# Optimization experiments

Hardware: AMD Instinct MI355X
Metric: run time of the kernel (lower is better)

The kernel has to match this reference:

```python
import jax, jax.numpy as jnp
import numpy as np

N_NODES = 20000
N_EDGES = 640000
NODE_NF = 64
HIDDEN = 256
N_LAYERS = 4


def _linear_init(key, fan_in, fan_out, layers=None):
    shape = (fan_in, fan_out) if layers is None else (layers, fan_in, fan_out)
    scale = 1.0 / np.sqrt(fan_in)
    return jax.random.normal(key, shape, dtype=jnp.float32) * scale


def setup_inputs() -> dict:
    key = jax.random.key(0)
    ks = jax.random.split(key, 16)
    L, H = N_LAYERS, HIDDEN
    return {
        "h": jax.random.normal(ks[0], (N_NODES, NODE_NF), dtype=jnp.float32),
        "edge_index": jax.random.randint(ks[1], (2, N_EDGES), 0, N_NODES, dtype=jnp.int64),
        "coord_diff": jax.random.normal(ks[2], (N_EDGES, 3), dtype=jnp.float32),
        # embedding in / out
        "w_in": _linear_init(ks[3], NODE_NF, H),
        "b_in": jnp.zeros((H,), jnp.float32),
        "w_out": _linear_init(ks[4], H, NODE_NF),
        "b_out": jnp.zeros((NODE_NF,), jnp.float32),
        # per-layer edge MLP: Linear(2H+1 -> H), silu, Linear(H -> H), silu
        "edge_w1": _linear_init(ks[5], 2 * H + 1, H, L),
        "edge_b1": jnp.zeros((L, H), jnp.float32),
        "edge_w2": _linear_init(ks[6], H, H, L),
        "edge_b2": jnp.zeros((L, H), jnp.float32),
        # per-layer node MLP: Linear(2H -> H), silu, Linear(H -> H)
        "node_w1": _linear_init(ks[7], 2 * H, H, L),
        "node_b1": jnp.zeros((L, H), jnp.float32),
        "node_w2": _linear_init(ks[8], H, H, L),
        "node_b2": jnp.zeros((L, H), jnp.float32),
    }


def reference(h, edge_index, coord_diff, w_in, b_in, w_out, b_out,
              edge_w1, edge_b1, edge_w2, edge_b2,
              node_w1, node_b1, node_w2, node_b2):
    row, col = edge_index[0], edge_index[1]
    # radial is layer-independent: [E, 1]
    radial = jnp.sum(coord_diff ** 2, axis=1, keepdims=True)

    h = h @ w_in + b_in  # [N, H]
    n_nodes = h.shape[0]

    for l in range(N_LAYERS):
        # edge model: gather endpoints, concat with radial, 2-layer MLP
        m = jnp.concatenate([h[row], h[col], radial], axis=1)  # [E, 2H+1]
        m = jax.nn.silu(m @ edge_w1[l] + edge_b1[l])
        m = jax.nn.silu(m @ edge_w2[l] + edge_b2[l])  # [E, H]
        # node model: segment-sum aggregate over row, concat, 2-layer MLP
        agg = jax.ops.segment_sum(m, row, num_segments=n_nodes)  # [N, H]
        x = jnp.concatenate([h, agg], axis=1)  # [N, 2H]
        x = jax.nn.silu(x @ node_w1[l] + node_b1[l])
        h = x @ node_w2[l] + node_b2[l]  # recurrent=False: no residual

    return h @ w_out + b_out  # [N, node_nf]
```

## Files before the change

### kernel.cpp

```cpp
#include <hip/hip_runtime.h>
#include <hip/hip_bf16.h>
#include <cstdint>
#include <cstddef>

#define NN 20000
#define NE 640000
#define NF 64
#define HD 256
#define NL 4
#define HTS 640

typedef __attribute__((ext_vector_type(8))) short short8;
typedef __attribute__((ext_vector_type(4))) float f32x4;
typedef __attribute__((ext_vector_type(2))) float f32x2;

__device__ __forceinline__ float bf2f(unsigned short u){
  union { unsigned int i; float f; } x; x.i = ((unsigned int)u) << 16; return x.f;
}
__device__ __forceinline__ unsigned short f2bf(float f){
  union { float f; unsigned int i; } x; x.f = f;
  unsigned int r = x.i + 0x7FFFu + ((x.i >> 16) & 1u);
  return (unsigned short)(r >> 16);
}
__device__ __forceinline__ unsigned int pk2bf(float a, float b){
  union { __hip_bfloat162 h; unsigned int u; } cv;
  cv.h = __float22bfloat162_rn(float2{a, b});
  return cv.u;
}
__device__ __forceinline__ float silu_f(float v){
  float e = __builtin_amdgcn_exp2f(v * -1.442695041f);
  return v * __builtin_amdgcn_rcpf(1.0f + e);
}
__device__ __forceinline__ f32x2 silu2(f32x2 v){
  f32x2 t = v * (f32x2){-1.442695041f, -1.442695041f};
  f32x2 e = (f32x2){__builtin_amdgcn_exp2f(t.x), __builtin_amdgcn_exp2f(t.y)};
  f32x2 d = e + (f32x2){1.0f, 1.0f};
  f32x2 r = (f32x2){__builtin_amdgcn_rcpf(d.x), __builtin_amdgcn_rcpf(d.y)};
  return v * r;
}
__device__ __forceinline__ void async16(const void* g, void* l){
  __builtin_amdgcn_global_load_lds(
      (const __attribute__((address_space(1))) unsigned int*)g,
      (__attribute__((address_space(3))) unsigned int*)l, 16, 0, 0);
}

__global__ __launch_bounds__(256) void prep_small(
    const float* __restrict__ w_in, const float* __restrict__ w_out,
    const float* __restrict__ ew1, const float* __restrict__ ew2,
    const float* __restrict__ nw1, const float* __restrict__ nw2,
    const float* __restrict__ eb1,
    unsigned short* __restrict__ w_in_t, unsigned short* __restrict__ w_out_t,
    unsigned short* __restrict__ ew1cat, float* __restrict__ w1r,
    float* __restrict__ b1e,
    unsigned short* __restrict__ ew2t, unsigned short* __restrict__ nw1t,
    unsigned short* __restrict__ nw2t)
{
  const int s = blockIdx.y;
  const int tid = blockIdx.x * 256 + threadIdx.x;
  if (s == 18) {
    if (tid < NL * 512) {
      int l = tid >> 9, c = tid & 511;
      b1e[tid] = (c < 256) ? eb1[l * HD + c] : 0.0f;
    }
    return;
  }
  if (s >= 2 && s < 6) {
    int l = s - 2;
    if (tid >= 513 * HD) return;
    int k = tid / HD, n = tid - k * HD;
    float v = ew1[(size_t)l * 513 * HD + tid];
    if (k == 512) { w1r[l * HD + n] = v; return; }
    unsigned short* dst = ew1cat + (size_t)l * 512 * 256;
    if (k < 256) dst[(size_t)n * 256 + k] = f2bf(v);
    else         dst[(size_t)(256 + n) * 256 + (k - 256)] = f2bf(v);
    return;
  }
  const float* src; unsigned short* dst; int K, N;
  if (s == 0)      { src = w_in;  dst = w_in_t;  K = NF;   N = HD; }
  else if (s == 1) { src = w_out; dst = w_out_t; K = HD;   N = NF; }
  else if (s < 10) { int l = s-6;  src = ew2 + (size_t)l*HD*HD;   dst = ew2t + (size_t)l*HD*HD;  K = HD;   N = HD; }
  else if (s < 14) { int l = s-10; src = nw1 + (size_t)l*2*HD*HD; dst = nw1t + (size_t)l*HD*512; K = 2*HD; N = HD; }
  else             { int l = s-14; src = nw2 + (size_t)l*HD*HD;   dst = nw2t + (size_t)l*HD*HD;  K = HD;   N = HD; }
  if (tid >= K * N) return;
  int k = tid / N, n = tid - k * N;
  dst[(size_t)n * K + k] = f2bf(src[tid]);
}

__global__ __launch_bounds__(256) void prep_big(
    const float* __restrict__ h_in, const float* __restrict__ cd,
    unsigned short* __restrict__ hb_in, float* __restrict__ radial)
{
  const int s = blockIdx.y;
  const int tid = blockIdx.x * 256 + threadIdx.x;
  if (s == 0) {
    if (tid < NN * NF) hb_in[tid] = f2bf(h_in[tid]);
  } else {
    if (tid < NE) {
      float x = cd[tid*3+0], y = cd[tid*3+1], z = cd[tid*3+2];
      radial[tid] = x*x + y*y + z*z;
    }
  }
}

__global__ __launch_bounds__(256) void hist_k(const int* __restrict__ erow, int* __restrict__ hist){
  int e = blockIdx.x * 256 + threadIdx.x;
  if (e < NE){
    unsigned r = (unsigned)erow[e]; if (r >= NN) r = 0;
    atomicAdd(&hist[r], 1);
  }
}

__global__ __launch_bounds__(256) void scan_k(const int* __restrict__ hist,
                                              int* __restrict__ starts, int* __restrict__ cursor){
  __shared__ int part[256];
  const int t = threadIdx.x;
  const int CH = 79;
  int lo = t * CH, hi = lo + CH; if (hi > NN) hi = NN; if (lo > NN) lo = NN;
  int s = 0;
  for (int i = lo; i < hi; ++i) s += hist[i];
  part[t] = s; __syncthreads();
  for (int off = 1; off < 256; off <<= 1){
    int v = (t >= off) ? part[t - off] : 0;
    __syncthreads();
    part[t] += v;
    __syncthreads();
  }
  int base = (t == 0) ? 0 : part[t - 1];
  for (int i = lo; i < hi; ++i){ starts[i] = base; cursor[i] = base; base += hist[i]; }
  if (t == 255) starts[NN] = part[255];
}

__global__ __launch_bounds__(256) void scatter_k(const int* __restrict__ erow,
                                                 const int* __restrict__ ecol,
                                                 const float* __restrict__ radial,
                                                 int* __restrict__ cursor,
                                                 int* __restrict__ rowcol,
                                                 float* __restrict__ radial_s){
  int e = blockIdx.x * 256 + threadIdx.x;
  if (e < NE){
    unsigned r = (unsigned)erow[e]; if (r >= NN) r = 0;
    unsigned c = (unsigned)ecol[e]; if (c >= NN) c = 0;
    int pos = atomicAdd(&cursor[r], 1);
    rowcol[2*pos]   = (int)r;
    rowcol[2*pos+1] = (int)c;
    radial_s[pos] = radial[e];
  }
}

__global__ __launch_bounds__(256) void gemm_k(
    const unsigned short* __restrict__ Am, const unsigned short* __restrict__ Wt,
    const float* __restrict__ bias,
    unsigned short* __restrict__ outB, float* __restrict__ outF,
    unsigned short* __restrict__ outB2,
    int M, int N, int K, int lda, int ldc, int fuseSilu)
{
  __shared__ __align__(16) unsigned short As[128*32];
  __shared__ __align__(16) unsigned short Bs[128*32];
  const int t = threadIdx.x;
  const int lane = t & 63, wave = t >> 6;
  const int ln15 = lane & 15, q = lane >> 4;
  const int bm = blockIdx.x, bn = blockIdx.y;
  const int wm = wave >> 1, wn = wave & 1;

  f32x4 acc[4][4];
  #pragma unroll
  for (int i = 0; i < 4; ++i)
    #pragma unroll
    for (int j = 0; j < 4; ++j) acc[i][j] = (f32x4){0.f,0.f,0.f,0.f};

  const int sr = t >> 2;
  const int sc = (t & 3) * 8;
  int am0 = bm*128 + sr;      if (am0 > M-1) am0 = M-1;
  int am1 = bm*128 + 64 + sr; if (am1 > M-1) am1 = M-1;
  int an0 = bn*128 + sr;      if (an0 > N-1) an0 = N-1;
  int an1 = bn*128 + 64 + sr; if (an1 > N-1) an1 = N-1;
  const unsigned short* a0 = Am + (size_t)am0 * lda + sc;
  const unsigned short* a1 = Am + (size_t)am1 * lda + sc;
  const unsigned short* b0 = Wt + (size_t)an0 * K + sc;
  const unsigned short* b1 = Wt + (size_t)an1 * K + sc;

  const int nkt = K >> 5;
  for (int kt = 0; kt < nkt; ++kt) {
    const int k0 = kt * 32;
    async16(a0 + k0, &As[t*8]);
    async16(a1 + k0, &As[2048 + t*8]);
    async16(b0 + k0, &Bs[t*8]);
    async16(b1 + k0, &Bs[2048 + t*8]);
    __syncthreads();
    short8 fa[4], fb[4];
    #pragma unroll
    for (int i = 0; i < 4; ++i)
      fa[i] = *(const short8*)&As[(wm*64 + i*16 + ln15)*32 + q*8];
    #pragma unroll
    for (int j = 0; j < 4; ++j)
      fb[j] = *(const short8*)&Bs[(wn*64 + j*16 + ln15)*32 + q*8];
    #pragma unroll
    for (int i = 0; i < 4; ++i)
      #pragma unroll
      for (int j = 0; j < 4; ++j)
        acc[i][j] = __builtin_amdgcn_mfma_f32_16x16x32_bf16(fa[i], fb[j], acc[i][j], 0, 0, 0);
    __syncthreads();
  }

  #pragma unroll
  for (int i = 0; i < 4; ++i) {
    #pragma unroll
    for (int j = 0; j < 4; ++j) {
      const int n = bn*128 + wn*64 + j*16 + ln15;
      if (n >= N) continue;
      const float bv = bias ? bias[n] : 0.0f;
      #pragma unroll
      for (int r = 0; r < 4; ++r) {
        const int m = bm*128 + wm*64 + i*16 + q*4 + r;
        if (m >= M) continue;
        float v = acc[i][j][r] + bv;
        if (fuseSilu) v = silu_f(v);
        if (outB) {
          unsigned short b = f2bf(v);
          outB[(size_t)m * ldc + n] = b;
          if (outB2 && n < 256) outB2[(size_t)m * 512 + n] = b;
        }
        else outF[(size_t)m * ldc + n] = v;
      }
    }
  }
}

__global__ __launch_bounds__(256, 4) void edge_k(
    const unsigned short* __restrict__ hT,
    const int* __restrict__ rowcol,
    const float* __restrict__ radial_s,
    const float* __restrict__ w1r,
    const unsigned short* __restrict__ w2t,
    const float* __restrict__ b2,
    float* __restrict__ agg)
{
  __shared__ __align__(16) unsigned short MBUF[16896];
  __shared__ int   rowS[64];
  __shared__ float w1rS[256];
  unsigned short* M1  = MBUF;
  unsigned short* m2T = MBUF;

  const int t = threadIdx.x;
  const int lane = t & 63, wave = t >> 6;
  const int ln15 = lane & 15, q = lane >> 4;
  int blk = blockIdx.x;
  blk = (blk & 7) * ((int)gridDim.x >> 3) + (blk >> 3);
  const int e0 = blk * 64;
  const int sr = t >> 2;
  const int sc_swz = (((t & 3) ^ ((sr >> 1) & 3))) * 8;
  const int xq = ((q ^ ((ln15 >> 1) & 3))) * 8;

  const int2 rc = *(const int2*)(rowcol + 2*(e0 + sr));
  int rowv = 0;
  if (t < 64) rowv = rowcol[2*(e0 + t)];
  const float w1v = w1r[t];
  const float rad = radial_s[e0 + sr];

  float bv2[4];
  #pragma unroll
  for (int j = 0; j < 4; ++j) bv2[j] = b2[wave*64 + j*16 + ln15];

  const unsigned short* hr = hT + (size_t)rc.x * HTS + sc_swz;
  const unsigned short* hc = hT + (size_t)rc.y * HTS + 256 + sc_swz;

  short8 va[8], vb[8];
  #pragma unroll
  for (int ch = 0; ch < 8; ++ch) {
    va[ch] = *(const short8*)(hr + ch*32);
    vb[ch] = *(const short8*)(hc + ch*32);
  }

  if (t < 64) rowS[t] = rowv;
  w1rS[t] = w1v;

  const unsigned short* w2row[4];
  #pragma unroll
  for (int j = 0; j < 4; ++j)
    w2row[j] = w2t + (size_t)(wave*64 + j*16 + ln15) * HD + q*8;

  __syncthreads();

  const f32x2 rad2 = (f32x2){rad, rad};
  #pragma unroll
  for (int ch = 0; ch < 8; ++ch) {
    const int c0 = ch*32 + sc_swz;
    const unsigned int* ua = (const unsigned int*)&va[ch];
    const unsigned int* ub = (const unsigned int*)&vb[ch];
    union { unsigned int u[4]; short8 s; } res;
    #pragma unroll
    for (int i = 0; i < 4; ++i) {
      union { unsigned int i; float f; } alo, ahi, blo, bhi;
      alo.i = ua[i] << 16; ahi.i = ua[i] & 0xFFFF0000u;
      blo.i = ub[i] << 16; bhi.i = ub[i] & 0xFFFF0000u;
      f32x2 av = (f32x2){alo.f, ahi.f};
      f32x2 bv = (f32x2){blo.f, bhi.f};
      f32x2 wv = *(const f32x2*)&w1rS[c0 + 2*i];
      f32x2 o = av + bv;
      o = o + rad2 * wv;
      f32x2 sv = silu2(o);
      res.u[i] = pk2bf(sv.x, sv.y);
    }
    *(short8*)&M1[ch*2048 + sr*32 + (t & 3)*8] = res.s;
  }
  __syncthreads();

  f32x4 acc2[4][4];
  #pragma unroll
  for (int i = 0; i < 4; ++i)
    #pragma unroll
    for (int j = 0; j < 4; ++j) acc2[i][j] = (f32x4){0.f,0.f,0.f,0.f};

  __builtin_amdgcn_s_setprio(1);
  #pragma unroll
  for (int kt = 0; kt < 8; ++kt) {
    short8 fa[4], fb[4];
    #pragma unroll
    for (int j = 0; j < 4; ++j) fb[j] = *(const short8*)(w2row[j] + kt*32);
    #pragma unroll
    for (int i = 0; i < 4; ++i) fa[i] = *(const short8*)&M1[kt*2048 + (i*16 + ln15)*32 + xq];
    #pragma unroll
    for (int i = 0; i < 4; ++i)
      #pragma unroll
      for (int j = 0; j < 4; ++j)
        acc2[i][j] = __builtin_amdgcn_mfma_f32_16x16x32_bf16(fa[i], fb[j], acc2[i][j], 0, 0, 0);
  }
  __builtin_amdgcn_s_setprio(0);
  __syncthreads();

  #pragma unroll
  for (int i = 0; i < 4; ++i) {
    #pragma unroll
    for (int j = 0; j < 4; ++j) {
      const int n = wave*64 + j*16 + ln15;
      const f32x2 b2v = (f32x2){bv2[j], bv2[j]};
      f32x2 s01 = (f32x2){acc2[i][j][0], acc2[i][j][1]} + b2v;
      f32x2 s23 = (f32x2){acc2[i][j][2], acc2[i][j][3]} + b2v;
      f32x2 r01 = silu2(s01);
      f32x2 r23 = silu2(s23);
      const int m = i*16 + q*4;
      *(unsigned int*)&m2T[n*66 + m]     = pk2bf(r01.x, r01.y);
      *(unsigned int*)&m2T[n*66 + m + 2] = pk2bf(r23.x, r23.y);
    }
  }
  __syncthreads();

  {
    const int c = t;
    int cur = __builtin_amdgcn_readfirstlane(rowS[0]);
    float s = 0.f;
    #pragma unroll
    for (int m = 0; m < 64; m += 4) {
      unsigned int u0 = *(const unsigned int*)&m2T[c*66 + m];
      unsigned int u1 = *(const unsigned int*)&m2T[c*66 + m + 2];
      int n0 = __builtin_amdgcn_readfirstlane(rowS[m]);
      int n1 = __builtin_amdgcn_readfirstlane(rowS[m+1]);
      int n2 = __builtin_amdgcn_readfirstlane(rowS[m+2]);
      int n3 = __builtin_amdgcn_readfirstlane(rowS[m+3]);
      float f0 = bf2f((unsigned short)u0), f1 = bf2f((unsigned short)(u0 >> 16));
      float f2v = bf2f((unsigned short)u1), f3 = bf2f((unsigned short)(u1 >> 16));
      if (n0 != cur) { atomicAdd(&agg[(size_t)cur * HD + c], s); s = 0.f; cur = n0; }
      s += f0;
      if (n1 != cur) { atomicAdd(&agg[(size_t)cur * HD + c], s); s = 0.f; cur = n1; }
      s += f1;
      if (n2 != cur) { atomicAdd(&agg[(size_t)cur * HD + c], s); s = 0.f; cur = n2; }
      s += f2v;
      if (n3 != cur) { atomicAdd(&agg[(size_t)cur * HD + c], s); s = 0.f; cur = n3; }
      s += f3;
    }
    atomicAdd(&agg[(size_t)cur * HD + c], s);
  }
}

__global__ __launch_bounds__(256) void aggcvt_k(
    float* __restrict__ agg, unsigned short* __restrict__ xcat)
{
  const int g = blockIdx.x * 256 + threadIdx.x;
  const int node = g >> 6;
  const int c = (g & 63) * 4;
  if (node >= NN) return;
  float4 a = *(const float4*)(agg + (size_t)node * HD + c);
  uint2 pk; pk.x = pk2bf(a.x, a.y); pk.y = pk2bf(a.z, a.w);
  *(uint2*)(xcat + (size_t)node * 2 * HD + HD + c) = pk;
  *(float4*)(agg + (size_t)node * HD + c) = float4{0.f, 0.f, 0.f, 0.f};
}

extern "C" void kernel_launch(void* const* d_in, const int* in_sizes, int n_in,
                              void* d_out, int out_size, void* d_ws, size_t ws_size,
                              hipStream_t stream)
{
  (void)in_sizes; (void)n_in; (void)out_size; (void)ws_size;
  const float* h_in  = (const float*)d_in[0];
  const int*   ei    = (const int*)d_in[1];
  const float* cd    = (const float*)d_in[2];
  const float* w_in  = (const float*)d_in[3];
  const float* b_in  = (const float*)d_in[4];
  const float* w_out = (const float*)d_in[5];
  const float* b_out = (const float*)d_in[6];
  const float* ew1   = (const float*)d_in[7];
  const float* eb1   = (const float*)d_in[8];
  const float* ew2   = (const float*)d_in[9];
  const float* eb2   = (const float*)d_in[10];
  const float* nw1   = (const float*)d_in[11];
  const float* nb1   = (const float*)d_in[12];
  const float* nw2   = (const float*)d_in[13];
  const float* nb2   = (const float*)d_in[14];
  float* out = (float*)d_out;

  char* base = (char*)d_ws;
  size_t off = 0;
  auto WS = [&](size_t bytes) -> char* {
    char* p = base + off;
    off = (off + bytes + 255) & ~(size_t)255;
    return p;
  };
  float*          radial  = (float*)WS((size_t)NE * 4);
  unsigned short* hb_in   = (unsigned short*)WS((size_t)NN * NF * 2);
  unsigned short* hcur    = (unsigned short*)WS((size_t)NN * HD * 2);
  unsigned short* xcat    = (unsigned short*)WS((size_t)NN * 2 * HD * 2);
  float*          aggF    = (float*)WS((size_t)NN * HD * 4);
  unsigned short* hT      = (unsigned short*)WS((size_t)NN * HTS * 2);
  unsigned short* x1      = hT;
  unsigned short* w_in_t  = (unsigned short*)WS((size_t)NF * HD * 2);
  unsigned short* w_out_t = (unsigned short*)WS((size_t)NF * HD * 2);
  unsigned short* ew1cat  = (unsigned short*)WS((size_t)NL * 512 * 256 * 2);
  float*          w1r     = (float*)WS((size_t)NL * HD * 4);
  float*          b1e     = (float*)WS((size_t)NL * 512 * 4);
  unsigned short* ew2t    = (unsigned short*)WS((size_t)NL * HD * HD * 2);
  unsigned short* nw1t    = (unsigned short*)WS((size_t)NL * HD * 512 * 2);
  unsigned short* nw2t    = (unsigned short*)WS((size_t)NL * HD * HD * 2);
  int*            hist    = (int*)WS((size_t)NN * 4);
  int*            starts  = (int*)WS((size_t)(NN + 1) * 4);
  int*            cursor  = (int*)WS((size_t)NN * 4);
  int*            rowcol  = (int*)WS((size_t)NE * 2 * 4);
  float*          radial_s= (float*)WS((size_t)NE * 4);

  hipMemsetAsync(hist, 0, (size_t)NN * 4, stream);
  hipMemsetAsync(aggF, 0, (size_t)NN * HD * 4, stream);
  prep_small<<<dim3(513, 19), 256, 0, stream>>>(w_in, w_out, ew1, ew2, nw1, nw2, eb1,
      w_in_t, w_out_t, ew1cat, w1r, b1e, ew2t, nw1t, nw2t);
  prep_big<<<dim3(5000, 2), 256, 0, stream>>>(h_in, cd, hb_in, radial);
  hist_k<<<NE / 256, 256, 0, stream>>>(ei, hist);
  scan_k<<<1, 256, 0, stream>>>(hist, starts, cursor);
  scatter_k<<<NE / 256, 256, 0, stream>>>(ei, ei + NE, radial, cursor, rowcol, radial_s);

  gemm_k<<<dim3(157, 2), 256, 0, stream>>>(hb_in, w_in_t, b_in, hcur, nullptr, xcat,
      NN, HD, NF, NF, HD, 0);

  for (int l = 0; l < NL; ++l) {
    gemm_k<<<dim3(157, 4), 256, 0, stream>>>(hcur, ew1cat + (size_t)l * 512 * 256,
        b1e + (size_t)l * 512, hT, nullptr, nullptr, NN, 512, HD, HD, HTS, 0);
    edge_k<<<NE / 64, 256, 0, stream>>>(hT, rowcol, radial_s,
        w1r + l * HD, ew2t + (size_t)l * HD * HD, eb2 + l * HD, aggF);
    aggcvt_k<<<NN * 64 / 256, 256, 0, stream>>>(aggF, xcat);
    gemm_k<<<dim3(157, 2), 256, 0, stream>>>(xcat, nw1t + (size_t)l * HD * 512,
        nb1 + l * HD, x1, nullptr, nullptr, NN, HD, 2 * HD, 2 * HD, HD, 1);
    gemm_k<<<dim3(157, 2), 256, 0, stream>>>(x1, nw2t + (size_t)l * HD * HD,
        nb2 + l * HD, hcur, nullptr, (l < NL-1) ? xcat : nullptr, NN, HD, HD, HD, HD, 0);
  }

  gemm_k<<<dim3(157, 1), 256, 0, stream>>>(hcur, w_out_t, b_out, nullptr, out, nullptr,
      NN, NF, HD, HD, NF, 0);
}
```

Measured before the change: 1.356 ms.

## Halve edge tile to 32 edges per block to raise occupancy

Each edge_k block now handles 32 edges instead of 64. Shared memory and register use shrink, the occupancy hint rises from 4 to 5 blocks per CU, and twice as many blocks are launched. The per-edge gather layout is reorganised so each thread loads 4 swizzled chunks for one edge. The radial weights are read straight from global memory instead of being staged in shared memory, which drops one barrier. In exchange, each block reloads the full W2 weight fragments for only half as many edges, and the segmented atomic reduction flushes more partial sums at block boundaries.

New measurement: 1.938 ms. +42.9%, slower.

```diff
diff --git a/kernel.cpp b/kernel.cpp
--- a/kernel.cpp
+++ b/kernel.cpp
@@ -9,6 +9,7 @@
 #define HD 256
 #define NL 4
 #define HTS 640
+#define EB 32
 
 typedef __attribute__((ext_vector_type(8))) short short8;
 typedef __attribute__((ext_vector_type(4))) float f32x4;
@@ -226,7 +227,7 @@
   }
 }
 
-__global__ __launch_bounds__(256, 4) void edge_k(
+__global__ __launch_bounds__(256, 5) void edge_k(
     const unsigned short* __restrict__ hT,
     const int* __restrict__ rowcol,
     const float* __restrict__ radial_s,
@@ -235,9 +236,8 @@
     const float* __restrict__ b2,
     float* __restrict__ agg)
 {
-  __shared__ __align__(16) unsigned short MBUF[16896];
-  __shared__ int   rowS[64];
-  __shared__ float w1rS[256];
+  __shared__ __align__(16) unsigned short MBUF[8704];
+  __shared__ int rowS[EB];
   unsigned short* M1  = MBUF;
   unsigned short* m2T = MBUF;
 
@@ -246,81 +246,80 @@
   const int ln15 = lane & 15, q = lane >> 4;
   int blk = blockIdx.x;
   blk = (blk & 7) * ((int)gridDim.x >> 3) + (blk >> 3);
-  const int e0 = blk * 64;
-  const int sr = t >> 2;
-  const int sc_swz = (((t & 3) ^ ((sr >> 1) & 3))) * 8;
-  const int xq = ((q ^ ((ln15 >> 1) & 3))) * 8;
-
-  const int2 rc = *(const int2*)(rowcol + 2*(e0 + sr));
-  int rowv = 0;
-  if (t < 64) rowv = rowcol[2*(e0 + t)];
-  const float w1v = w1r[t];
-  const float rad = radial_s[e0 + sr];
+  const int e0 = blk * EB;
+  const int e = t & 31;
+  const int u = t >> 5;
+  const int s = (e >> 1) & 3;
+  const int xq = (q ^ ((ln15 >> 1) & 3)) * 8;
+
+  const int2 rc = *(const int2*)(rowcol + 2*(e0 + e));
+  const float rad = radial_s[e0 + e];
+  if (t < EB) rowS[t] = rc.x;
 
   float bv2[4];
   #pragma unroll
   for (int j = 0; j < 4; ++j) bv2[j] = b2[wave*64 + j*16 + ln15];
 
-  const unsigned short* hr = hT + (size_t)rc.x * HTS + sc_swz;
-  const unsigned short* hc = hT + (size_t)rc.y * HTS + 256 + sc_swz;
-
-  short8 va[8], vb[8];
-  #pragma unroll
-  for (int ch = 0; ch < 8; ++ch) {
-    va[ch] = *(const short8*)(hr + ch*32);
-    vb[ch] = *(const short8*)(hc + ch*32);
-  }
-
-  if (t < 64) rowS[t] = rowv;
-  w1rS[t] = w1v;
+  const unsigned short* hr = hT + (size_t)rc.x * HTS + u*32;
+  const unsigned short* hc = hT + (size_t)rc.y * HTS + 256 + u*32;
+  const float* w1g = w1r + u*32;
+
+  short8 va[4], vb[4];
+  #pragma unroll
+  for (int p = 0; p < 4; ++p) {
+    const int g = (p ^ s) * 8;
+    va[p] = *(const short8*)(hr + g);
+    vb[p] = *(const short8*)(hc + g);
+  }
 
   const unsigned short* w2row[4];
   #pragma unroll
   for (int j = 0; j < 4; ++j)
     w2row[j] = w2t + (size_t)(wave*64 + j*16 + ln15) * HD + q*8;
 
-  __syncthreads();
-
   const f32x2 rad2 = (f32x2){rad, rad};
   #pragma unroll
-  for (int ch = 0; ch < 8; ++ch) {
-    const int c0 = ch*32 + sc_swz;
-    const unsigned int* ua = (const unsigned int*)&va[ch];
-    const unsigned int* ub = (const unsigned int*)&vb[ch];
-    union { unsigned int u[4]; short8 s; } res;
-    #pragma unroll
-    for (int i = 0; i < 4; ++i) {
+  for (int p = 0; p < 4; ++p) {
+    const int g = (p ^ s) * 8;
+    f32x4 w0 = *(const f32x4*)(w1g + g);
+    f32x4 w1v = *(const f32x4*)(w1g + g + 4);
+    float wArr[8] = {w0[0], w0[1], w0[2], w0[3], w1v[0], w1v[1], w1v[2], w1v[3]};
+    const unsigned int* ua = (const unsigned int*)&va[p];
+    const unsigned int* ub = (const unsigned int*)&vb[p];
+    union { unsigned int u[4]; short8 s8; } res;
+    #pragma unroll
+    for (int i2 = 0; i2 < 4; ++i2) {
       union { unsigned int i; float f; } alo, ahi, blo, bhi;
-      alo.i = ua[i] << 16; ahi.i = ua[i] & 0xFFFF0000u;
-      blo.i = ub[i] << 16; bhi.i = ub[i] & 0xFFFF0000u;
+      alo.i = ua[i2] << 16; ahi.i = ua[i2] & 0xFFFF0000u;
+      blo.i = ub[i2] << 16; bhi.i = ub[i2] & 0xFFFF0000u;
       f32x2 av = (f32x2){alo.f, ahi.f};
       f32x2 bv = (f32x2){blo.f, bhi.f};
-      f32x2 wv = *(const f32x2*)&w1rS[c0 + 2*i];
+      f32x2 wv = (f32x2){wArr[2*i2], wArr[2*i2+1]};
       f32x2 o = av + bv;
       o = o + rad2 * wv;
       f32x2 sv = silu2(o);
-      res.u[i] = pk2bf(sv.x, sv.y);
-    }
-    *(short8*)&M1[ch*2048 + sr*32 + (t & 3)*8] = res.s;
+      res.u[i2] = pk2bf(sv.x, sv.y);
+    }
+    *(short8*)&M1[u*1024 + e*32 + p*8] = res.s8;
   }
   __syncthreads();
 
-  f32x4 acc2[4][4];
-  #pragma unroll
-  for (int i = 0; i < 4; ++i)
+  f32x4 acc2[2][4];
+  #pragma unroll
+  for (int i = 0; i < 2; ++i)
     #pragma unroll
     for (int j = 0; j < 4; ++j) acc2[i][j] = (f32x4){0.f,0.f,0.f,0.f};
 
   __builtin_amdgcn_s_setprio(1);
   #pragma unroll
   for (int kt = 0; kt < 8; ++kt) {
-    short8 fa[4], fb[4];
+    short8 fa[2], fb[4];
     #pragma unroll
     for (int j = 0; j < 4; ++j) fb[j] = *(const short8*)(w2row[j] + kt*32);
     #pragma unroll
-    for (int i = 0; i < 4; ++i) fa[i] = *(const short8*)&M1[kt*2048 + (i*16 + ln15)*32 + xq];
-    #pragma unroll
-    for (int i = 0; i < 4; ++i)
+    for (int i = 0; i < 2; ++i) fa[i] = *(const short8*)&M1[kt*1024 + (i*16 + ln15)*32 + xq];
+    #pragma unroll
+    for (int i = 0; i < 2; ++i)
       #pragma unroll
       for (int j = 0; j < 4; ++j)
         acc2[i][j] = __builtin_amdgcn_mfma_f32_16x16x32_bf16(fa[i], fb[j], acc2[i][j], 0, 0, 0);
@@ -329,7 +328,7 @@
   __syncthreads();
 
   #pragma unroll
-  for (int i = 0; i < 4; ++i) {
+  for (int i = 0; i < 2; ++i) {
     #pragma unroll
     for (int j = 0; j < 4; ++j) {
       const int n = wave*64 + j*16 + ln15;
@@ -339,8 +338,8 @@
       f32x2 r01 = silu2(s01);
       f32x2 r23 = silu2(s23);
       const int m = i*16 + q*4;
-      *(unsigned int*)&m2T[n*66 + m]     = pk2bf(r01.x, r01.y);
-      *(unsigned int*)&m2T[n*66 + m + 2] = pk2bf(r23.x, r23.y);
+      *(unsigned int*)&m2T[n*34 + m]     = pk2bf(r01.x, r01.y);
+      *(unsigned int*)&m2T[n*34 + m + 2] = pk2bf(r23.x, r23.y);
     }
   }
   __syncthreads();
@@ -348,27 +347,27 @@
   {
     const int c = t;
     int cur = __builtin_amdgcn_readfirstlane(rowS[0]);
-    float s = 0.f;
-    #pragma unroll
-    for (int m = 0; m < 64; m += 4) {
-      unsigned int u0 = *(const unsigned int*)&m2T[c*66 + m];
-      unsigned int u1 = *(const unsigned int*)&m2T[c*66 + m + 2];
+    float sacc = 0.f;
+    #pragma unroll
+    for (int m = 0; m < EB; m += 4) {
+      unsigned int u0 = *(const unsigned int*)&m2T[c*34 + m];
+      unsigned int u1 = *(const unsigned int*)&m2T[c*34 + m + 2];
       int n0 = __builtin_amdgcn_readfirstlane(rowS[m]);
       int n1 = __builtin_amdgcn_readfirstlane(rowS[m+1]);
       int n2 = __builtin_amdgcn_readfirstlane(rowS[m+2]);
       int n3 = __builtin_amdgcn_readfirstlane(rowS[m+3]);
       float f0 = bf2f((unsigned short)u0), f1 = bf2f((unsigned short)(u0 >> 16));
       float f2v = bf2f((unsigned short)u1), f3 = bf2f((unsigned short)(u1 >> 16));
-      if (n0 != cur) { atomicAdd(&agg[(size_t)cur * HD + c], s); s = 0.f; cur = n0; }
-      s += f0;
-      if (n1 != cur) { atomicAdd(&agg[(size_t)cur * HD + c], s); s = 0.f; cur = n1; }
-      s += f1;
-      if (n2 != cur) { atomicAdd(&agg[(size_t)cur * HD + c], s); s = 0.f; cur = n2; }
-      s += f2v;
-      if (n3 != cur) { atomicAdd(&agg[(size_t)cur * HD + c], s); s = 0.f; cur = n3; }
-      s += f3;
-    }
-    atomicAdd(&agg[(size_t)cur * HD + c], s);
+      if (n0 != cur) { atomicAdd(&agg[(size_t)cur * HD + c], sacc); sacc = 0.f; cur = n0; }
+      sacc += f0;
+      if (n1 != cur) { atomicAdd(&agg[(size_t)cur * HD + c], sacc); sacc = 0.f; cur = n1; }
+      sacc += f1;
+      if (n2 != cur) { atomicAdd(&agg[(size_t)cur * HD + c], sacc); sacc = 0.f; cur = n2; }
+      sacc += f2v;
+      if (n3 != cur) { atomicAdd(&agg[(size_t)cur * HD + c], sacc); sacc = 0.f; cur = n3; }
+      sacc += f3;
+    }
+    atomicAdd(&agg[(size_t)cur * HD + c], sacc);
   }
 }
 
@@ -450,7 +449,7 @@
   for (int l = 0; l < NL; ++l) {
     gemm_k<<<dim3(157, 4), 256, 0, stream>>>(hcur, ew1cat + (size_t)l * 512 * 256,
         b1e + (size_t)l * 512, hT, nullptr, nullptr, NN, 512, HD, HD, HTS, 0);
-    edge_k<<<NE / 64, 256, 0, stream>>>(hT, rowcol, radial_s,
+    edge_k<<<NE / EB, 256, 0, stream>>>(hT, rowcol, radial_s,
         w1r + l * HD, ew2t + (size_t)l * HD * HD, eb2 + l * HD, aggF);
     aggcvt_k<<<NN * 64 / 256, 256, 0, stream>>>(aggF, xcat);
     gemm_k<<<dim3(157, 2), 256, 0, stream>>>(xcat, nw1t + (size_t)l * HD * 512,
```

## Segment-reduce edge messages with one-hot MFMA and XOR-swizzled transposed LDS tile

Applied to the files above, without the earlier changes.

When a block's 64 edges cover at most 16 consecutive destination rows, the edge kernel now builds a one-hot bf16 selector from the row indices. It multiplies that selector with the message tile using MFMA to get per-segment sums, then issues one atomicAdd per non-zero segment and column. This replaces the serial per-column scan over 64 edges. The transposed message buffer in shared memory moves from a padded stride of 66 to a 72-stride layout with XOR-swizzled 8-element chunks, so it supports 16-byte vector loads without bank conflicts. The old scan remains as a fallback for wider spans. The cost is slightly more shared memory per block and extra selector construction work.

After: 1.425 ms. 1.05x slower.

```diff
diff --git a/kernel.cpp b/kernel.cpp
--- a/kernel.cpp
+++ b/kernel.cpp
@@ -235,8 +235,8 @@
     const float* __restrict__ b2,
     float* __restrict__ agg)
 {
-  __shared__ __align__(16) unsigned short MBUF[16896];
-  __shared__ int   rowS[64];
+  __shared__ __align__(16) unsigned short MBUF[18432];
+  __shared__ __align__(16) int rowS[64];
   __shared__ float w1rS[256];
   unsigned short* M1  = MBUF;
   unsigned short* m2T = MBUF;
@@ -339,20 +339,55 @@
       f32x2 r01 = silu2(s01);
       f32x2 r23 = silu2(s23);
       const int m = i*16 + q*4;
-      *(unsigned int*)&m2T[n*66 + m]     = pk2bf(r01.x, r01.y);
-      *(unsigned int*)&m2T[n*66 + m + 2] = pk2bf(r23.x, r23.y);
+      const int base = n*72 + (((m >> 3) ^ (n & 7)) << 3) + (m & 7);
+      *(unsigned int*)&m2T[base]     = pk2bf(r01.x, r01.y);
+      *(unsigned int*)&m2T[base + 2] = pk2bf(r23.x, r23.y);
     }
   }
   __syncthreads();
 
-  {
+  const int seg0 = __builtin_amdgcn_readfirstlane(rowS[0]);
+  const int rend = __builtin_amdgcn_readfirstlane(rowS[63]);
+  const int span = rend - seg0 + 1;
+  if (span <= 16) {
+    const int tgt = seg0 + ln15;
+    short8 sf[2];
+    #pragma unroll
+    for (int kt2 = 0; kt2 < 2; ++kt2) {
+      const int* rp = &rowS[kt2*32 + q*8];
+      short8 s8;
+      #pragma unroll
+      for (int i = 0; i < 8; ++i)
+        s8[i] = (short)((rp[i] == tgt) ? 0x3F80 : 0);
+      sf[kt2] = s8;
+    }
+    #pragma unroll
+    for (int ct = 0; ct < 4; ++ct) {
+      const int col = wave*64 + ct*16 + ln15;
+      f32x4 a3 = (f32x4){0.f,0.f,0.f,0.f};
+      #pragma unroll
+      for (int kt2 = 0; kt2 < 2; ++kt2) {
+        const int chunk = (kt2*4 + q) ^ (col & 7);
+        short8 bf = *(const short8*)&m2T[col*72 + chunk*8];
+        a3 = __builtin_amdgcn_mfma_f32_16x16x32_bf16(sf[kt2], bf, a3, 0, 0, 0);
+      }
+      #pragma unroll
+      for (int r = 0; r < 4; ++r) {
+        const int sgi = q*4 + r;
+        const float v = a3[r];
+        if (sgi < span && v != 0.0f)
+          atomicAdd(&agg[(size_t)(seg0 + sgi) * HD + col], v);
+      }
+    }
+  } else {
     const int c = t;
-    int cur = __builtin_amdgcn_readfirstlane(rowS[0]);
+    int cur = seg0;
     float s = 0.f;
     #pragma unroll
     for (int m = 0; m < 64; m += 4) {
-      unsigned int u0 = *(const unsigned int*)&m2T[c*66 + m];
-      unsigned int u1 = *(const unsigned int*)&m2T[c*66 + m + 2];
+      const int base = c*72 + (((m >> 3) ^ (c & 7)) << 3) + (m & 7);
+      unsigned int u0 = *(const unsigned int*)&m2T[base];
+      unsigned int u1 = *(const unsigned int*)&m2T[base + 2];
       int n0 = __builtin_amdgcn_readfirstlane(rowS[m]);
       int n1 = __builtin_amdgcn_readfirstlane(rowS[m+1]);
       int n2 = __builtin_amdgcn_readfirstlane(rowS[m+2]);
```

## Fuse node MLP, aggregate conversion and concat into one node kernel

Applied to the files above, without the earlier changes.

Replaces the aggcvt kernel and the two node-MLP GEMMs with a single node_k kernel. It reads hcur and the fp32 aggregate directly, converts and zeroes the aggregate in place, and keeps the silu hidden layer in LDS for the second GEMM. This drops the xcat concat buffer, the x1 round-trip through global memory and two launches per layer. In exchange it uses 64-row tiles with all 256 output columns per block, which gives about 313 blocks with larger LDS use and may lower occupancy or parallelism.

New measurement: 1.232 ms. -9.1%, faster.

```diff
diff --git a/kernel.cpp b/kernel.cpp
--- a/kernel.cpp
+++ b/kernel.cpp
@@ -151,7 +151,6 @@
     const unsigned short* __restrict__ Am, const unsigned short* __restrict__ Wt,
     const float* __restrict__ bias,
     unsigned short* __restrict__ outB, float* __restrict__ outF,
-    unsigned short* __restrict__ outB2,
     int M, int N, int K, int lda, int ldc, int fuseSilu)
 {
   __shared__ __align__(16) unsigned short As[128*32];
@@ -215,12 +214,137 @@
         if (m >= M) continue;
         float v = acc[i][j][r] + bv;
         if (fuseSilu) v = silu_f(v);
-        if (outB) {
-          unsigned short b = f2bf(v);
-          outB[(size_t)m * ldc + n] = b;
-          if (outB2 && n < 256) outB2[(size_t)m * 512 + n] = b;
-        }
-        else outF[(size_t)m * ldc + n] = v;
+        if (outB) outB[(size_t)m * ldc + n] = f2bf(v);
+        else      outF[(size_t)m * ldc + n] = v;
+      }
+    }
+  }
+}
+
+__global__ __launch_bounds__(256, 3) void node_k(
+    unsigned short* __restrict__ hcur,
+    float* __restrict__ aggF,
+    const unsigned short* __restrict__ w1t,
+    const float* __restrict__ b1,
+    const unsigned short* __restrict__ w2t,
+    const float* __restrict__ b2,
+    int M)
+{
+  __shared__ __align__(16) unsigned short As[64*32];
+  __shared__ __align__(16) unsigned short Bs[256*32];
+  __shared__ __align__(16) unsigned short x1L[8*64*32];
+  const int t = threadIdx.x;
+  const int lane = t & 63, wave = t >> 6;
+  const int ln15 = lane & 15, q = lane >> 4;
+  const int bm = blockIdx.x;
+  const int sr = t >> 2;
+  const int sc = (t & 3) * 8;
+
+  const int row = bm*64 + sr;
+  const int valid = (row < M);
+  const int rowc = valid ? row : (M - 1);
+  const unsigned short* aSrc = hcur + (size_t)rowc * HD + sc;
+  float* gSrc = aggF + (size_t)rowc * HD + sc;
+
+  float bv1[4], bv2[4];
+  #pragma unroll
+  for (int j = 0; j < 4; ++j) {
+    bv1[j] = b1[wave*64 + j*16 + ln15];
+    bv2[j] = b2[wave*64 + j*16 + ln15];
+  }
+
+  f32x4 acc[4][4];
+  #pragma unroll
+  for (int i = 0; i < 4; ++i)
+    #pragma unroll
+    for (int j = 0; j < 4; ++j) acc[i][j] = (f32x4){0.f,0.f,0.f,0.f};
+
+  for (int kt = 0; kt < 16; ++kt) {
+    if (kt < 8) {
+      async16(aSrc + kt*32, &As[t*8]);
+    } else {
+      union { unsigned int u[4]; short8 s8; } cv;
+      if (valid) {
+        float* p = gSrc + (kt-8)*32;
+        float4 a0 = *(const float4*)p;
+        float4 a1 = *(const float4*)(p + 4);
+        cv.u[0] = pk2bf(a0.x, a0.y); cv.u[1] = pk2bf(a0.z, a0.w);
+        cv.u[2] = pk2bf(a1.x, a1.y); cv.u[3] = pk2bf(a1.z, a1.w);
+        *(float4*)p = float4{0.f,0.f,0.f,0.f};
+        *(float4*)(p + 4) = float4{0.f,0.f,0.f,0.f};
+      } else {
+        cv.u[0] = cv.u[1] = cv.u[2] = cv.u[3] = 0u;
+      }
+      *(short8*)&As[t*8] = cv.s8;
+    }
+    #pragma unroll
+    for (int i = 0; i < 4; ++i)
+      async16(w1t + (size_t)(i*64 + sr) * 512 + kt*32 + sc, &Bs[i*2048 + t*8]);
+    __syncthreads();
+    short8 fa[4], fb[4];
+    #pragma unroll
+    for (int i = 0; i < 4; ++i) fa[i] = *(const short8*)&As[(i*16 + ln15)*32 + q*8];
+    #pragma unroll
+    for (int j = 0; j < 4; ++j) fb[j] = *(const short8*)&Bs[(wave*64 + j*16 + ln15)*32 + q*8];
+    #pragma unroll
+    for (int i = 0; i < 4; ++i)
+      #pragma unroll
+      for (int j = 0; j < 4; ++j)
+        acc[i][j] = __builtin_amdgcn_mfma_f32_16x16x32_bf16(fa[i], fb[j], acc[i][j], 0, 0, 0);
+    __syncthreads();
+  }
+
+  #pragma unroll
+  for (int i = 0; i < 4; ++i) {
+    #pragma unroll
+    for (int j = 0; j < 4; ++j) {
+      const int k = wave*64 + j*16 + ln15;
+      const int kt2 = k >> 5, k31 = k & 31;
+      const f32x2 b2v = (f32x2){bv1[j], bv1[j]};
+      f32x2 s01 = (f32x2){acc[i][j][0], acc[i][j][1]} + b2v;
+      f32x2 s23 = (f32x2){acc[i][j][2], acc[i][j][3]} + b2v;
+      f32x2 r01 = silu2(s01);
+      f32x2 r23 = silu2(s23);
+      const int r0 = i*16 + q*4;
+      x1L[kt2*2048 + (r0  )*32 + k31] = f2bf(r01.x);
+      x1L[kt2*2048 + (r0+1)*32 + k31] = f2bf(r01.y);
+      x1L[kt2*2048 + (r0+2)*32 + k31] = f2bf(r23.x);
+      x1L[kt2*2048 + (r0+3)*32 + k31] = f2bf(r23.y);
+    }
+  }
+  #pragma unroll
+  for (int i = 0; i < 4; ++i)
+    #pragma unroll
+    for (int j = 0; j < 4; ++j) acc[i][j] = (f32x4){0.f,0.f,0.f,0.f};
+
+  for (int kt2 = 0; kt2 < 8; ++kt2) {
+    #pragma unroll
+    for (int i = 0; i < 4; ++i)
+      async16(w2t + (size_t)(i*64 + sr) * 256 + kt2*32 + sc, &Bs[i*2048 + t*8]);
+    __syncthreads();
+    short8 fa[4], fb[4];
+    #pragma unroll
+    for (int i = 0; i < 4; ++i) fa[i] = *(const short8*)&x1L[kt2*2048 + (i*16 + ln15)*32 + q*8];
+    #pragma unroll
+    for (int j = 0; j < 4; ++j) fb[j] = *(const short8*)&Bs[(wave*64 + j*16 + ln15)*32 + q*8];
+    #pragma unroll
+    for (int i = 0; i < 4; ++i)
+      #pragma unroll
+      for (int j = 0; j < 4; ++j)
+        acc[i][j] = __builtin_amdgcn_mfma_f32_16x16x32_bf16(fa[i], fb[j], acc[i][j], 0, 0, 0);
+    __syncthreads();
+  }
+
+  #pragma unroll
+  for (int i = 0; i < 4; ++i) {
+    #pragma unroll
+    for (int j = 0; j < 4; ++j) {
+      const int n = wave*64 + j*16 + ln15;
+      #pragma unroll
+      for (int r = 0; r < 4; ++r) {
+        const int m = bm*64 + i*16 + q*4 + r;
+        if (m >= M) continue;
+        hcur[(size_t)m * HD + n] = f2bf(acc[i][j][r] + bv2[j]);
       }
     }
   }
@@ -370,19 +494,6 @@
     }
     atomicAdd(&agg[(size_t)cur * HD + c], s);
   }
-}
-
-__global__ __launch_bounds__(256) void aggcvt_k(
-    float* __restrict__ agg, unsigned short* __restrict__ xcat)
-{
-  const int g = blockIdx.x * 256 + threadIdx.x;
-  const int node = g >> 6;
-  const int c = (g & 63) * 4;
-  if (node >= NN) return;
-  float4 a = *(const float4*)(agg + (size_t)node * HD + c);
-  uint2 pk; pk.x = pk2bf(a.x, a.y); pk.y = pk2bf(a.z, a.w);
-  *(uint2*)(xcat + (size_t)node * 2 * HD + HD + c) = pk;
-  *(float4*)(agg + (size_t)node * HD + c) = float4{0.f, 0.f, 0.f, 0.f};
 }
 
 extern "C" void kernel_launch(void* const* d_in, const int* in_sizes, int n_in,
@@ -417,10 +528,8 @@
   float*          radial  = (float*)WS((size_t)NE * 4);
   unsigned short* hb_in   = (unsigned short*)WS((size_t)NN * NF * 2);
   unsigned short* hcur    = (unsigned short*)WS((size_t)NN * HD * 2);
-  unsigned short* xcat    = (unsigned short*)WS((size_t)NN * 2 * HD * 2);
   float*          aggF    = (float*)WS((size_t)NN * HD * 4);
   unsigned short* hT      = (unsigned short*)WS((size_t)NN * HTS * 2);
-  unsigned short* x1      = hT;
   unsigned short* w_in_t  = (unsigned short*)WS((size_t)NF * HD * 2);
   unsigned short* w_out_t = (unsigned short*)WS((size_t)NF * HD * 2);
   unsigned short* ew1cat  = (unsigned short*)WS((size_t)NL * 512 * 256 * 2);
@@ -444,21 +553,19 @@
   scan_k<<<1, 256, 0, stream>>>(hist, starts, cursor);
   scatter_k<<<NE / 256, 256, 0, stream>>>(ei, ei + NE, radial, cursor, rowcol, radial_s);
 
-  gemm_k<<<dim3(157, 2), 256, 0, stream>>>(hb_in, w_in_t, b_in, hcur, nullptr, xcat,
+  gemm_k<<<dim3(157, 2), 256, 0, stream>>>(hb_in, w_in_t, b_in, hcur, nullptr,
       NN, HD, NF, NF, HD, 0);
 
   for (int l = 0; l < NL; ++l) {
     gemm_k<<<dim3(157, 4), 256, 0, stream>>>(hcur, ew1cat + (size_t)l * 512 * 256,
-        b1e + (size_t)l * 512, hT, nullptr, nullptr, NN, 512, HD, HD, HTS, 0);
+        b1e + (size_t)l * 512, hT, nullptr, NN, 512, HD, HD, HTS, 0);
     edge_k<<<NE / 64, 256, 0, stream>>>(hT, rowcol, radial_s,
         w1r + l * HD, ew2t + (size_t)l * HD * HD, eb2 + l * HD, aggF);
-    aggcvt_k<<<NN * 64 / 256, 256, 0, stream>>>(aggF, xcat);
-    gemm_k<<<dim3(157, 2), 256, 0, stream>>>(xcat, nw1t + (size_t)l * HD * 512,
-        nb1 + l * HD, x1, nullptr, nullptr, NN, HD, 2 * HD, 2 * HD, HD, 1);
-    gemm_k<<<dim3(157, 2), 256, 0, stream>>>(x1, nw2t + (size_t)l * HD * HD,
-        nb2 + l * HD, hcur, nullptr, (l < NL-1) ? xcat : nullptr, NN, HD, HD, HD, HD, 0);
-  }
-
-  gemm_k<<<dim3(157, 1), 256, 0, stream>>>(hcur, w_out_t, b_out, nullptr, out, nullptr,
+    node_k<<<(NN + 63) / 64, 256, 0, stream>>>(hcur, aggF,
+        nw1t + (size_t)l * HD * 512, nb1 + l * HD,
+        nw2t + (size_t)l * HD * HD, nb2 + l * HD, NN);
+  }
+
+  gemm_k<<<dim3(157, 1), 256, 0, stream>>>(hcur, w_out_t, b_out, nullptr, out,
       NN, NF, HD, HD, NF, 0);
 }
```
